# Kernel optimization log

Measured on AMD Instinct MI355X. Metric: run time of the kernel, lower is better.

The kernel has to match this reference:

```python
import jax, jax.numpy as jnp
import numpy as np

B, T, E, H = 4, 2048, 1024, 16
D = E // H  # head dim = 64


def setup_inputs() -> dict:
    key = jax.random.key(0)
    k1, k2, k3 = jax.random.split(key, 3)
    g = jax.random.normal(k1, (B, T, E), dtype=jnp.float32)
    W_lift = jax.random.normal(k2, (2 * E, E), dtype=jnp.float32) * (1.0 / np.sqrt(E))
    W_proj = jax.random.normal(k3, (H, H), dtype=jnp.float32) * (1.0 / np.sqrt(H))
    return {"g": g, "W_lift": W_lift, "W_proj": W_proj}


def reference(g, W_lift, W_proj):
    b, t, e = g.shape
    h, d = H, e // H
    # lift: Linear(E, 2E, bias=False) -> split into q, k
    qk = jnp.einsum('bte,fe->btf', g, W_lift)  # (B, T, 2E)
    q, k = qk[..., :e], qk[..., e:]
    q = q.reshape(b, t, h, d).transpose(0, 2, 1, 3)  # (B, H, T, D)
    k = k.reshape(b, t, h, d).transpose(0, 2, 1, 3)  # (B, H, T, D)
    # unscaled causal scores
    a = jnp.einsum('bhqd,bhkd->bhqk', q, k)  # (B, H, T, T)
    causal = jnp.tril(jnp.ones((t, t), dtype=bool))
    a = jnp.where(causal[None, None], a, -jnp.inf)
    # masked logsumexp over key dim -> (B, H, T)
    lse = jax.scipy.special.logsumexp(a, axis=-1)
    out = lse.transpose(0, 2, 1)  # (B, T, H)
    out = jnp.einsum('bth,gh->btg', out, W_proj)  # proj Linear(H, H)
    out = out.sum(axis=2)  # (B, T)
    return out.reshape(-1, out.shape[-1])
```

## Files before the change

### kernel.cpp

```cpp
#include <hip/hip_runtime.h>
#include <hip/hip_bf16.h>

#define B_ 4
#define T_ 2048
#define E_ 1024
#define H_ 16
#define D_ 64
#define Mtot 8192
#define N2 2048
#define K_ 1024
#define PS_ (B_ * H_ * T_)
#define NKT 16

typedef __attribute__((ext_vector_type(8))) short short8;
typedef __attribute__((ext_vector_type(4))) float f32x4;
using bf16 = __hip_bfloat16;

__device__ __forceinline__ void async_copy16(const void* g, void* l) {
  __builtin_amdgcn_global_load_lds(
      (const __attribute__((address_space(1))) unsigned int*)g,
      (__attribute__((address_space(3))) unsigned int*)l, 16, 0, 0);
}

__global__ void cast_f32_to_bf16(const float* __restrict__ in, ushort* __restrict__ out, int n4) {
  int stride = gridDim.x * blockDim.x;
  for (int i = blockIdx.x * blockDim.x + threadIdx.x; i < n4; i += stride) {
    float4 v = reinterpret_cast<const float4*>(in)[i];
    bf16 a = __float2bfloat16(v.x), b = __float2bfloat16(v.y);
    bf16 c = __float2bfloat16(v.z), d = __float2bfloat16(v.w);
    ushort4 o = make_ushort4(*(ushort*)&a, *(ushort*)&b, *(ushort*)&c, *(ushort*)&d);
    reinterpret_cast<ushort4*>(out)[i] = o;
  }
}

#define MFMA_BF16(a, b, c) __builtin_amdgcn_mfma_f32_16x16x32_bf16(a, b, c, 0, 0, 0)

__launch_bounds__(512, 2)
__global__ void lift_gemm(const bf16* __restrict__ A, const bf16* __restrict__ Bm,
                          bf16* __restrict__ qh, bf16* __restrict__ kh) {
  __shared__ __align__(16) char sL[8][16384];
  const int bid = blockIdx.x;
  const int swz = ((bid & 7) << 5) | (bid >> 3);
  const int m0 = (swz >> 3) * 256;
  const int n0 = (swz & 7) * 256;
  const int tid = threadIdx.x;
  const int lane = tid & 63, w = tid >> 6;
  const int wm = w >> 2, wn = w & 3;
  const int lr = lane & 15, lg = lane >> 4;

  f32x4 acc[8][4];
#pragma unroll
  for (int i = 0; i < 8; ++i)
#pragma unroll
    for (int j = 0; j < 4; ++j) acc[i][j] = (f32x4)(0.0f);

  auto stage_half = [&](int slot, const bf16* gsrc, int Rbase, int kcol) {
#pragma unroll
    for (int it = 0; it < 2; ++it) {
      const int o = ((it * 512 + tid) << 4);
      const int lin = o ^ (((o >> 7) & 7) << 4);
      const int r = lin >> 7, cb = lin & 127;
      async_copy16((const char*)gsrc + ((size_t)(Rbase + r) * K_ + kcol) * 2 + cb,
                   &sL[slot][o]);
    }
  };
  auto rd = [&](int slot, int row, int khalf) -> short8 {
    int off = (row << 7) + (khalf << 6) + (lg << 4);
    off ^= (row & 7) << 4;
    return *(const short8*)&sL[slot][off];
  };

  stage_half(0, A, m0, 0);
  stage_half(1, A, m0 + 128, 0);
  stage_half(2, Bm, n0, 0);
  stage_half(3, Bm, n0 + 128, 0);

  short8 af[4][2], bf0[2][2], bf1[2][2];

  for (int kt = 0; kt < NKT; ++kt) {
    const int cb = (kt & 1) << 2;
    const int nb = cb ^ 4;
    const int kcol = (kt + 1) * 64;
    const int aslot = cb + wm;
    const int bslot = cb + 2 + (wn >> 1);
    const int brow = (wn & 1) * 64;

    if (kt + 1 < NKT) {
      stage_half(nb + 0, A, m0, kcol);
      stage_half(nb + 1, A, m0 + 128, kcol);
      asm volatile("s_waitcnt vmcnt(4)" ::: "memory");
    } else {
      asm volatile("s_waitcnt vmcnt(0)" ::: "memory");
    }
    __builtin_amdgcn_sched_barrier(0);
    __builtin_amdgcn_s_barrier();
#pragma unroll
    for (int i = 0; i < 4; ++i) {
      af[i][0] = rd(aslot, i * 16 + lr, 0);
      af[i][1] = rd(aslot, i * 16 + lr, 1);
    }
#pragma unroll
    for (int j = 0; j < 2; ++j) {
      bf0[j][0] = rd(bslot, brow + j * 16 + lr, 0);
      bf0[j][1] = rd(bslot, brow + j * 16 + lr, 1);
    }
    __builtin_amdgcn_s_setprio(1);
#pragma unroll
    for (int i = 0; i < 4; ++i)
#pragma unroll
      for (int j = 0; j < 2; ++j) {
        acc[i][j] = MFMA_BF16(af[i][0], bf0[j][0], acc[i][j]);
        acc[i][j] = MFMA_BF16(af[i][1], bf0[j][1], acc[i][j]);
      }
    __builtin_amdgcn_s_setprio(0);
    __builtin_amdgcn_sched_barrier(0);
    __builtin_amdgcn_s_barrier();

    if (kt + 1 < NKT) {
      stage_half(nb + 2, Bm, n0, kcol);
      stage_half(nb + 3, Bm, n0 + 128, kcol);
    }
#pragma unroll
    for (int j = 0; j < 2; ++j) {
      bf1[j][0] = rd(bslot, brow + (j + 2) * 16 + lr, 0);
      bf1[j][1] = rd(bslot, brow + (j + 2) * 16 + lr, 1);
    }
    __builtin_amdgcn_sched_barrier(0);
    __builtin_amdgcn_s_barrier();
    __builtin_amdgcn_s_setprio(1);
#pragma unroll
    for (int i = 0; i < 4; ++i)
#pragma unroll
      for (int j = 0; j < 2; ++j) {
        acc[i][j + 2] = MFMA_BF16(af[i][0], bf1[j][0], acc[i][j + 2]);
        acc[i][j + 2] = MFMA_BF16(af[i][1], bf1[j][1], acc[i][j + 2]);
      }
    __builtin_amdgcn_s_setprio(0);
    __builtin_amdgcn_sched_barrier(0);
    __builtin_amdgcn_s_barrier();

#pragma unroll
    for (int i = 0; i < 4; ++i) {
      af[i][0] = rd(aslot, (i + 4) * 16 + lr, 0);
      af[i][1] = rd(aslot, (i + 4) * 16 + lr, 1);
    }
    __builtin_amdgcn_sched_barrier(0);
    __builtin_amdgcn_s_barrier();
    __builtin_amdgcn_s_setprio(1);
#pragma unroll
    for (int i = 0; i < 4; ++i)
#pragma unroll
      for (int j = 0; j < 2; ++j) {
        acc[i + 4][j] = MFMA_BF16(af[i][0], bf0[j][0], acc[i + 4][j]);
        acc[i + 4][j] = MFMA_BF16(af[i][1], bf0[j][1], acc[i + 4][j]);
      }
    __builtin_amdgcn_s_setprio(0);
    __builtin_amdgcn_sched_barrier(0);
    __builtin_amdgcn_s_barrier();

    __builtin_amdgcn_s_setprio(1);
#pragma unroll
    for (int i = 0; i < 4; ++i)
#pragma unroll
      for (int j = 0; j < 2; ++j) {
        acc[i + 4][j + 2] = MFMA_BF16(af[i][0], bf1[j][0], acc[i + 4][j + 2]);
        acc[i + 4][j + 2] = MFMA_BF16(af[i][1], bf1[j][1], acc[i + 4][j + 2]);
      }
    __builtin_amdgcn_s_setprio(0);
    __builtin_amdgcn_sched_barrier(0);
    __builtin_amdgcn_s_barrier();
  }

#pragma unroll
  for (int mi = 0; mi < 8; ++mi) {
#pragma unroll
    for (int ni = 0; ni < 4; ++ni) {
#pragma unroll
      for (int r = 0; r < 4; ++r) {
        int m = m0 + wm * 128 + mi * 16 + lg * 4 + r;
        int f = n0 + wn * 64 + ni * 16 + lr;
        bf16 bv = __float2bfloat16(acc[mi][ni][r]);
        int b = m >> 11, t = m & (T_ - 1);
        int hh = (f & (E_ - 1)) >> 6, d = f & (D_ - 1);
        bf16* dst = (f < E_) ? qh : kh;
        dst[((((size_t)b * H_ + hh) * T_) + t) * D_ + d] = bv;
      }
    }
  }
}

#define LSE_QT 128

__launch_bounds__(256)
__global__ void attn_lse(const bf16* __restrict__ qh, const bf16* __restrict__ kh,
                         float* __restrict__ psum) {
  __shared__ __align__(16) bf16 sK[2][64 * 64];
  const int bid = blockIdx.x;
  const int qt = 15 - (bid >> 8);
  const int rem = bid & 255;
  const int bh = rem >> 2;
  const int s = rem & 3;
  const int tid = threadIdx.x;
  const int lane = tid & 63, w = tid >> 6;
  const int lr = lane & 15, lg = lane >> 4;
  const int qbase = qt * LSE_QT + w * 32;

  const bf16* qp = qh + ((size_t)bh * T_ + qbase) * D_;
  short8 qf[2][2];
#pragma unroll
  for (int f = 0; f < 2; ++f)
#pragma unroll
    for (int h = 0; h < 2; ++h)
      qf[f][h] = *(const short8*)&qp[(size_t)(f * 16 + lr) * D_ + h * 32 + lg * 8];

  float l[2][4];
#pragma unroll
  for (int f = 0; f < 2; ++f)
#pragma unroll
    for (int r = 0; r < 4; ++r) l[f][r] = 0.0f;

  const char* kbase = (const char*)(kh + (size_t)bh * T_ * D_);
  const int nfullw = qt * 2 + (w >> 1);
  const int maxk = qt * 2 + 1;
  const int nt = (s <= maxk) ? ((maxk - s) >> 2) + 1 : 0;

#define STAGE_K(bi, kt_)                                                      \
  do {                                                                        \
    const char* kp_ = kbase + (size_t)(kt_) * (64 * D_ * 2);                  \
    _Pragma("unroll") for (int it = 0; it < 2; ++it) {                        \
      const int o = ((w * 2 + it) << 10) | (lane << 4);                       \
      const int lin = o ^ (((o >> 7) & 7) << 4);                              \
      async_copy16(kp_ + lin, (char*)&sK[bi][0] + ((w * 2 + it) << 10));      \
    }                                                                         \
  } while (0)

  int cur = 0;
  if (nt > 0) STAGE_K(0, s);
  for (int i = 0; i < nt; ++i) {
    __syncthreads();
    if (i + 1 < nt) STAGE_K(cur ^ 1, s + 4 * (i + 1));
    const int kt = s + 4 * i;
    if (kt <= nfullw) {
      const char* kb = (const char*)&sK[cur][0];
      short8 kf[4][2];
#pragma unroll
      for (int j = 0; j < 4; ++j) {
        int row = j * 16 + lr;
        int sw = ((row & 7) << 4);
        kf[j][0] = *(const short8*)(kb + (((row << 7) | (lg << 4)) ^ sw));
        kf[j][1] = *(const short8*)(kb + (((row << 7) | 64 | (lg << 4)) ^ sw));
      }
      f32x4 sc[2][4];
#pragma unroll
      for (int f = 0; f < 2; ++f)
#pragma unroll
        for (int j = 0; j < 4; ++j) sc[f][j] = (f32x4)(0.0f);
#pragma unroll
      for (int j = 0; j < 4; ++j) {
        sc[0][j] = MFMA_BF16(qf[0][0], kf[j][0], sc[0][j]);
        sc[0][j] = MFMA_BF16(qf[0][1], kf[j][1], sc[0][j]);
        sc[1][j] = MFMA_BF16(qf[1][0], kf[j][0], sc[1][j]);
        sc[1][j] = MFMA_BF16(qf[1][1], kf[j][1], sc[1][j]);
      }
      if (kt < nfullw) {
#pragma unroll
        for (int f = 0; f < 2; ++f)
#pragma unroll
          for (int j = 0; j < 4; ++j)
#pragma unroll
            for (int r = 0; r < 4; ++r) l[f][r] += __expf(sc[f][j][r]);
      } else {
#pragma unroll
        for (int f = 0; f < 2; ++f)
#pragma unroll
          for (int j = 0; j < 4; ++j)
#pragma unroll
            for (int r = 0; r < 4; ++r) {
              int qrow = qbase + f * 16 + lg * 4 + r;
              int key = kt * 64 + j * 16 + lr;
              float a = (key <= qrow) ? sc[f][j][r] : -INFINITY;
              l[f][r] += __expf(a);
            }
      }
    }
    __syncthreads();
    cur ^= 1;
  }

#pragma unroll
  for (int f = 0; f < 2; ++f)
#pragma unroll
    for (int r = 0; r < 4; ++r) {
      float v = l[f][r];
      v += __shfl_xor(v, 1);
      v += __shfl_xor(v, 2);
      v += __shfl_xor(v, 4);
      v += __shfl_xor(v, 8);
      if (lr == 0)
        psum[(size_t)s * PS_ + (size_t)bh * T_ + qbase + f * 16 + lg * 4 + r] = v;
    }
}

__global__ void proj_out(const float* __restrict__ psum, const float* __restrict__ Wp,
                         float* __restrict__ out) {
  __shared__ float cw[H_];
  int tid = threadIdx.x;
  if (tid < H_) {
    float s = 0.0f;
    for (int g = 0; g < H_; ++g) s += Wp[g * H_ + tid];
    cw[tid] = s;
  }
  __syncthreads();
  int idx = blockIdx.x * blockDim.x + tid;
  int b = idx >> 11, t = idx & (T_ - 1);
  float acc = 0.0f;
#pragma unroll
  for (int h = 0; h < H_; ++h) {
    size_t base = ((size_t)(b * H_ + h) * T_) + t;
    float v = psum[base] + psum[PS_ + base] + psum[2 * (size_t)PS_ + base] +
              psum[3 * (size_t)PS_ + base];
    acc += __logf(v) * cw[h];
  }
  out[idx] = acc;
}

extern "C" void kernel_launch(void* const* d_in, const int* in_sizes, int n_in,
                              void* d_out, int out_size, void* d_ws, size_t ws_size,
                              hipStream_t stream) {
  (void)in_sizes; (void)n_in; (void)out_size; (void)ws_size;
  const float* g  = (const float*)d_in[0];
  const float* Wl = (const float*)d_in[1];
  const float* Wp = (const float*)d_in[2];
  float* out = (float*)d_out;

  char* ws = (char*)d_ws;
  size_t off = 0;
  bf16* g_bf  = (bf16*)(ws + off); off += (size_t)Mtot * K_ * 2;
  bf16* wl_bf = (bf16*)(ws + off); off += (size_t)N2 * K_ * 2;
  bf16* qh    = (bf16*)(ws + off); off += (size_t)B_ * H_ * T_ * D_ * 2;
  bf16* kh    = (bf16*)(ws + off); off += (size_t)B_ * H_ * T_ * D_ * 2;
  float* psum = (float*)(ws + off);

  cast_f32_to_bf16<<<2048, 256, 0, stream>>>(g,  (ushort*)g_bf,  (Mtot * K_) / 4);
  cast_f32_to_bf16<<<512,  256, 0, stream>>>(Wl, (ushort*)wl_bf, (N2 * K_) / 4);

  lift_gemm<<<256, 512, 0, stream>>>(g_bf, wl_bf, qh, kh);

  attn_lse<<<4096, 256, 0, stream>>>(qh, kh, psum);

  proj_out<<<(B_ * T_) / 256, 256, 0, stream>>>(psum, Wp, out);
}
```

Measured before the change: 92.01 us.

## Enlarge attention LSE tiles to 256 query rows and 128-key K blocks

The attn_lse kernel now gives each block 256 query rows (64 per wave) and stages 128-key K tiles, halving the grid to 2048 blocks. Each K fragment read from LDS is reused across four query fragments instead of two, and in the diagonal tile the key sub-blocks that lie fully above the causal boundary are skipped. This is meant to cut LDS traffic, K reloads and barrier count per unit of work. The cost is more registers per thread, double the LDS per block, fewer blocks, and coarser load balance across the causal triangle.

```diff
diff --git a/kernel.cpp b/kernel.cpp
--- a/kernel.cpp
+++ b/kernel.cpp
@@ -189,50 +189,54 @@
   }
 }
 
-#define LSE_QT 128
-
 __launch_bounds__(256)
 __global__ void attn_lse(const bf16* __restrict__ qh, const bf16* __restrict__ kh,
                          float* __restrict__ psum) {
-  __shared__ __align__(16) bf16 sK[2][64 * 64];
+  __shared__ __align__(16) char sK[2][16384];
   const int bid = blockIdx.x;
-  const int qt = 15 - (bid >> 8);
+  const int qt = 7 - (bid >> 8);
   const int rem = bid & 255;
   const int bh = rem >> 2;
   const int s = rem & 3;
   const int tid = threadIdx.x;
   const int lane = tid & 63, w = tid >> 6;
   const int lr = lane & 15, lg = lane >> 4;
-  const int qbase = qt * LSE_QT + w * 32;
+  const int qbase = qt * 256 + w * 64;
 
   const bf16* qp = qh + ((size_t)bh * T_ + qbase) * D_;
-  short8 qf[2][2];
-#pragma unroll
-  for (int f = 0; f < 2; ++f)
+  short8 qf[4][2];
+#pragma unroll
+  for (int fi = 0; fi < 4; ++fi)
 #pragma unroll
     for (int h = 0; h < 2; ++h)
-      qf[f][h] = *(const short8*)&qp[(size_t)(f * 16 + lr) * D_ + h * 32 + lg * 8];
-
-  float l[2][4];
-#pragma unroll
-  for (int f = 0; f < 2; ++f)
-#pragma unroll
-    for (int r = 0; r < 4; ++r) l[f][r] = 0.0f;
+      qf[fi][h] = *(const short8*)&qp[(size_t)(fi * 16 + lr) * D_ + h * 32 + lg * 8];
+
+  float l[4][4];
+#pragma unroll
+  for (int fi = 0; fi < 4; ++fi)
+#pragma unroll
+    for (int r = 0; r < 4; ++r) l[fi][r] = 0.0f;
 
   const char* kbase = (const char*)(kh + (size_t)bh * T_ * D_);
-  const int nfullw = qt * 2 + (w >> 1);
-  const int maxk = qt * 2 + 1;
+  const int nfullw = qbase >> 7;
+  const int maxk = 2 * qt + 1;
   const int nt = (s <= maxk) ? ((maxk - s) >> 2) + 1 : 0;
 
 #define STAGE_K(bi, kt_)                                                      \
   do {                                                                        \
-    const char* kp_ = kbase + (size_t)(kt_) * (64 * D_ * 2);                  \
-    _Pragma("unroll") for (int it = 0; it < 2; ++it) {                        \
-      const int o = ((w * 2 + it) << 10) | (lane << 4);                       \
+    const char* kp_ = kbase + (size_t)(kt_) * (128 * D_ * 2);                 \
+    _Pragma("unroll") for (int it = 0; it < 4; ++it) {                        \
+      const int o = ((it * 256 + tid) << 4);                                  \
       const int lin = o ^ (((o >> 7) & 7) << 4);                              \
-      async_copy16(kp_ + lin, (char*)&sK[bi][0] + ((w * 2 + it) << 10));      \
+      async_copy16(kp_ + lin, &sK[bi][o]);                                    \
     }                                                                         \
   } while (0)
+
+  auto krd = [&](const char* kb, int row, int khalf) -> short8 {
+    int off = (row << 7) + (khalf << 6) + (lg << 4);
+    off ^= (row & 7) << 4;
+    return *(const short8*)(kb + off);
+  };
 
   int cur = 0;
   if (nt > 0) STAGE_K(0, s);
@@ -240,47 +244,45 @@
     __syncthreads();
     if (i + 1 < nt) STAGE_K(cur ^ 1, s + 4 * (i + 1));
     const int kt = s + 4 * i;
-    if (kt <= nfullw) {
-      const char* kb = (const char*)&sK[cur][0];
-      short8 kf[4][2];
-#pragma unroll
-      for (int j = 0; j < 4; ++j) {
-        int row = j * 16 + lr;
-        int sw = ((row & 7) << 4);
-        kf[j][0] = *(const short8*)(kb + (((row << 7) | (lg << 4)) ^ sw));
-        kf[j][1] = *(const short8*)(kb + (((row << 7) | 64 | (lg << 4)) ^ sw));
-      }
-      f32x4 sc[2][4];
-#pragma unroll
-      for (int f = 0; f < 2; ++f)
-#pragma unroll
-        for (int j = 0; j < 4; ++j) sc[f][j] = (f32x4)(0.0f);
-#pragma unroll
-      for (int j = 0; j < 4; ++j) {
-        sc[0][j] = MFMA_BF16(qf[0][0], kf[j][0], sc[0][j]);
-        sc[0][j] = MFMA_BF16(qf[0][1], kf[j][1], sc[0][j]);
-        sc[1][j] = MFMA_BF16(qf[1][0], kf[j][0], sc[1][j]);
-        sc[1][j] = MFMA_BF16(qf[1][1], kf[j][1], sc[1][j]);
-      }
-      if (kt < nfullw) {
-#pragma unroll
-        for (int f = 0; f < 2; ++f)
-#pragma unroll
-          for (int j = 0; j < 4; ++j)
-#pragma unroll
-            for (int r = 0; r < 4; ++r) l[f][r] += __expf(sc[f][j][r]);
-      } else {
-#pragma unroll
-        for (int f = 0; f < 2; ++f)
-#pragma unroll
-          for (int j = 0; j < 4; ++j)
+    const char* kb = &sK[cur][0];
+    if (kt < nfullw) {
+#pragma unroll
+      for (int j = 0; j < 8; ++j) {
+        short8 k0 = krd(kb, j * 16 + lr, 0);
+        short8 k1 = krd(kb, j * 16 + lr, 1);
+        f32x4 sc[4];
+#pragma unroll
+        for (int fi = 0; fi < 4; ++fi) {
+          sc[fi] = MFMA_BF16(qf[fi][0], k0, (f32x4)(0.0f));
+          sc[fi] = MFMA_BF16(qf[fi][1], k1, sc[fi]);
+        }
+#pragma unroll
+        for (int fi = 0; fi < 4; ++fi)
+#pragma unroll
+          for (int r = 0; r < 4; ++r) l[fi][r] += __expf(sc[fi][r]);
+      }
+    } else if (kt == nfullw) {
+#pragma unroll
+      for (int j = 0; j < 8; ++j) {
+        if (kt * 128 + j * 16 <= qbase + 63) {
+          short8 k0 = krd(kb, j * 16 + lr, 0);
+          short8 k1 = krd(kb, j * 16 + lr, 1);
+          f32x4 sc[4];
+#pragma unroll
+          for (int fi = 0; fi < 4; ++fi) {
+            sc[fi] = MFMA_BF16(qf[fi][0], k0, (f32x4)(0.0f));
+            sc[fi] = MFMA_BF16(qf[fi][1], k1, sc[fi]);
+          }
+          int key = kt * 128 + j * 16 + lr;
+#pragma unroll
+          for (int fi = 0; fi < 4; ++fi)
 #pragma unroll
             for (int r = 0; r < 4; ++r) {
-              int qrow = qbase + f * 16 + lg * 4 + r;
-              int key = kt * 64 + j * 16 + lr;
-              float a = (key <= qrow) ? sc[f][j][r] : -INFINITY;
-              l[f][r] += __expf(a);
+              int qrow = qbase + fi * 16 + lg * 4 + r;
+              float a = (key <= qrow) ? sc[fi][r] : -INFINITY;
+              l[fi][r] += __expf(a);
             }
+        }
       }
     }
     __syncthreads();
@@ -288,16 +290,16 @@
   }
 
 #pragma unroll
-  for (int f = 0; f < 2; ++f)
+  for (int fi = 0; fi < 4; ++fi)
 #pragma unroll
     for (int r = 0; r < 4; ++r) {
-      float v = l[f][r];
+      float v = l[fi][r];
       v += __shfl_xor(v, 1);
       v += __shfl_xor(v, 2);
       v += __shfl_xor(v, 4);
       v += __shfl_xor(v, 8);
       if (lr == 0)
-        psum[(size_t)s * PS_ + (size_t)bh * T_ + qbase + f * 16 + lg * 4 + r] = v;
+        psum[(size_t)s * PS_ + (size_t)bh * T_ + qbase + fi * 16 + lg * 4 + r] = v;
     }
 }
 
@@ -346,7 +348,7 @@
 
   lift_gemm<<<256, 512, 0, stream>>>(g_bf, wl_bf, qh, kh);
 
-  attn_lse<<<4096, 256, 0, stream>>>(qh, kh, psum);
+  attn_lse<<<2048, 256, 0, stream>>>(qh, kh, psum);
 
   proj_out<<<(B_ * T_) / 256, 256, 0, stream>>>(psum, Wp, out);
 }
```

Measured after the change: 100.5 us. +9.2%, slower.

## Fold log2e into Q and use exp2 with finer-grained async K waits

Applied to the files above, without the earlier changes.

The GEMM epilogue now scales the q half by log2(e) before the bf16 cast, so the attention kernel can use the native exp2 instruction instead of __expf, which needs an extra multiply. The K double-buffer loop now issues the next tile's async copy before the barrier and waits with an explicit vmcnt, so the prefetch overlaps the current tile instead of sitting behind a full syncthreads. Scaling before the bf16 rounding slightly changes the numerics of q, and the hand-written vmcnt counts assume exactly two outstanding loads per thread.

```diff
diff --git a/kernel.cpp b/kernel.cpp
--- a/kernel.cpp
+++ b/kernel.cpp
@@ -11,6 +11,7 @@
 #define K_ 1024
 #define PS_ (B_ * H_ * T_)
 #define NKT 16
+#define LOG2E 1.4426950408889634f
 
 typedef __attribute__((ext_vector_type(8))) short short8;
 typedef __attribute__((ext_vector_type(4))) float f32x4;
@@ -171,6 +172,7 @@
     __builtin_amdgcn_s_barrier();
   }
 
+  const float qscale = (n0 < E_) ? LOG2E : 1.0f;
 #pragma unroll
   for (int mi = 0; mi < 8; ++mi) {
 #pragma unroll
@@ -179,7 +181,7 @@
       for (int r = 0; r < 4; ++r) {
         int m = m0 + wm * 128 + mi * 16 + lg * 4 + r;
         int f = n0 + wn * 64 + ni * 16 + lr;
-        bf16 bv = __float2bfloat16(acc[mi][ni][r]);
+        bf16 bv = __float2bfloat16(acc[mi][ni][r] * qscale);
         int b = m >> 11, t = m & (T_ - 1);
         int hh = (f & (E_ - 1)) >> 6, d = f & (D_ - 1);
         bf16* dst = (f < E_) ? qh : kh;
@@ -194,7 +196,7 @@
 __launch_bounds__(256)
 __global__ void attn_lse(const bf16* __restrict__ qh, const bf16* __restrict__ kh,
                          float* __restrict__ psum) {
-  __shared__ __align__(16) bf16 sK[2][64 * 64];
+  __shared__ __align__(16) char sK[2][8192];
   const int bid = blockIdx.x;
   const int qt = 15 - (bid >> 8);
   const int rem = bid & 255;
@@ -220,8 +222,8 @@
     for (int r = 0; r < 4; ++r) l[f][r] = 0.0f;
 
   const char* kbase = (const char*)(kh + (size_t)bh * T_ * D_);
-  const int nfullw = qt * 2 + (w >> 1);
-  const int maxk = qt * 2 + 1;
+  const int nfullw = qbase >> 6;
+  const int maxk = 2 * qt + 1;
   const int nt = (s <= maxk) ? ((maxk - s) >> 2) + 1 : 0;
 
 #define STAGE_K(bi, kt_)                                                      \
@@ -234,21 +236,32 @@
     }                                                                         \
   } while (0)
 
+  auto krd = [&](const char* kb, int row, int khalf) -> short8 {
+    int off = (row << 7) + (khalf << 6) + (lg << 4);
+    off ^= (row & 7) << 4;
+    return *(const short8*)(kb + off);
+  };
+
   int cur = 0;
   if (nt > 0) STAGE_K(0, s);
   for (int i = 0; i < nt; ++i) {
-    __syncthreads();
-    if (i + 1 < nt) STAGE_K(cur ^ 1, s + 4 * (i + 1));
+    if (i + 1 < nt) {
+      STAGE_K(cur ^ 1, s + 4 * (i + 1));
+      asm volatile("s_waitcnt vmcnt(2)" ::: "memory");
+    } else {
+      asm volatile("s_waitcnt vmcnt(0)" ::: "memory");
+    }
+    __builtin_amdgcn_sched_barrier(0);
+    __builtin_amdgcn_s_barrier();
+
     const int kt = s + 4 * i;
     if (kt <= nfullw) {
-      const char* kb = (const char*)&sK[cur][0];
+      const char* kb = &sK[cur][0];
       short8 kf[4][2];
 #pragma unroll
       for (int j = 0; j < 4; ++j) {
-        int row = j * 16 + lr;
-        int sw = ((row & 7) << 4);
-        kf[j][0] = *(const short8*)(kb + (((row << 7) | (lg << 4)) ^ sw));
-        kf[j][1] = *(const short8*)(kb + (((row << 7) | 64 | (lg << 4)) ^ sw));
+        kf[j][0] = krd(kb, j * 16 + lr, 0);
+        kf[j][1] = krd(kb, j * 16 + lr, 1);
       }
       f32x4 sc[2][4];
 #pragma unroll
@@ -268,7 +281,8 @@
 #pragma unroll
           for (int j = 0; j < 4; ++j)
 #pragma unroll
-            for (int r = 0; r < 4; ++r) l[f][r] += __expf(sc[f][j][r]);
+            for (int r = 0; r < 4; ++r)
+              l[f][r] += __builtin_amdgcn_exp2f(sc[f][j][r]);
       } else {
 #pragma unroll
         for (int f = 0; f < 2; ++f)
@@ -279,11 +293,12 @@
               int qrow = qbase + f * 16 + lg * 4 + r;
               int key = kt * 64 + j * 16 + lr;
               float a = (key <= qrow) ? sc[f][j][r] : -INFINITY;
-              l[f][r] += __expf(a);
+              l[f][r] += __builtin_amdgcn_exp2f(a);
             }
       }
     }
-    __syncthreads();
+    __builtin_amdgcn_sched_barrier(0);
+    __builtin_amdgcn_s_barrier();
     cur ^= 1;
   }
 
```

Result: faster. 88.35 us (median of 2 runs) (-4.0%).
